# Kernel optimization log

Measured on AMD Instinct MI355X. Metric: run time of the kernel, lower is better.

## Reference

```python
import jax, jax.numpy as jnp
import numpy as np

NEG_SLOPE = 0.2
EPS = 1e-16  # PyG softmax denominator epsilon


def gat_conv(x, src, dst, W, att_src, att_dst, bias, concat):
    """One PyG-style GATConv layer (eval mode, self-loops already in src/dst).
    x: [N, F_in]; src/dst: [E]; W: [F_in, H*C]; att_*: [H, C]; bias: [H*C] or [C].
    """
    N = x.shape[0]
    H, C = att_src.shape
    h = (x @ W).reshape(N, H, C)                        # [N,H,C]
    a_s = jnp.sum(h * att_src[None], axis=-1)           # [N,H]
    a_d = jnp.sum(h * att_dst[None], axis=-1)           # [N,H]
    alpha = jax.nn.leaky_relu(a_s[src] + a_d[dst], NEG_SLOPE)  # [E,H]
    # segment softmax over incoming edges of each destination node
    m = jax.ops.segment_max(alpha, dst, num_segments=N)        # [N,H]
    alpha = jnp.exp(alpha - m[dst])
    denom = jax.ops.segment_sum(alpha, dst, num_segments=N)    # [N,H]
    alpha = alpha / (denom[dst] + EPS)
    # attention dropout is identity in eval mode
    out = jax.ops.segment_sum(h[src] * alpha[:, :, None], dst, num_segments=N)  # [N,H,C]
    out = out.reshape(N, H * C) if concat else out.mean(axis=1)
    return out + bias


def setup_inputs() -> dict:
    key = jax.random.key(0)
    ks = jax.random.split(key, 10)
    N, E, F_in, H, C1, F_out = 100000, 1600000, 128, 4, 32, 64
    hid = H * C1
    x = jax.random.normal(ks[0], (N, F_in), dtype=jnp.float32)
    edge_index = jax.random.randint(ks[1], (2, E), 0, N, dtype=jnp.int64)
    s = 1.0 / np.sqrt(F_in)
    W1 = jax.random.uniform(ks[2], (F_in, hid), minval=-s, maxval=s, dtype=jnp.float32)
    att_src1 = jax.random.normal(ks[3], (H, C1), dtype=jnp.float32) * 0.1
    att_dst1 = jax.random.normal(ks[4], (H, C1), dtype=jnp.float32) * 0.1
    b1 = jnp.zeros((hid,), dtype=jnp.float32)
    s2 = 1.0 / np.sqrt(hid)
    W2 = jax.random.uniform(ks[5], (hid, F_out), minval=-s2, maxval=s2, dtype=jnp.float32)
    att_src2 = jax.random.normal(ks[6], (1, F_out), dtype=jnp.float32) * 0.1
    att_dst2 = jax.random.normal(ks[7], (1, F_out), dtype=jnp.float32) * 0.1
    b2 = jnp.zeros((F_out,), dtype=jnp.float32)
    return {"x": x, "edge_index": edge_index,
            "W1": W1, "att_src1": att_src1, "att_dst1": att_dst1, "b1": b1,
            "W2": W2, "att_src2": att_src2, "att_dst2": att_dst2, "b2": b2}


def reference(x, edge_index, W1, att_src1, att_dst1, b1, W2, att_src2, att_dst2, b2):
    N = x.shape[0]
    loops = jnp.arange(N, dtype=edge_index.dtype)
    src = jnp.concatenate([edge_index[0], loops])  # add_self_loops=True (PyG default)
    dst = jnp.concatenate([edge_index[1], loops])
    h = gat_conv(x, src, dst, W1, att_src1, att_dst1, b1, concat=True)
    h = jax.nn.relu(h)  # dropout is identity in eval mode
    return gat_conv(h, src, dst, W2, att_src2, att_dst2, b2, concat=False)
```

## Files before the change

### kernel.cpp

```cpp
#include <hip/hip_runtime.h>
#include <hip/hip_bf16.h>

#define DEV static __device__ __forceinline__

typedef __attribute__((ext_vector_type(4))) float f32x4;
typedef __attribute__((ext_vector_type(8))) short bf16x8;
typedef __attribute__((ext_vector_type(8))) _Float16 half8;
typedef __attribute__((ext_vector_type(2))) _Float16 half2v;
typedef __attribute__((ext_vector_type(8))) unsigned short u16x8;

DEV float leakys(float v) { return v > 0.f ? v : 0.2f * v; }
DEV float4 add4(float4 a, float4 b) { return make_float4(a.x+b.x, a.y+b.y, a.z+b.z, a.w+b.w); }
DEV float4 leaky4(float4 v) { return make_float4(leakys(v.x), leakys(v.y), leakys(v.z), leakys(v.w)); }
DEV float4 exp4(float4 v) { return make_float4(__expf(v.x), __expf(v.y), __expf(v.z), __expf(v.w)); }
DEV float pick4(float4 v, int i) {
    float r = v.x;
    r = (i == 1) ? v.y : r;
    r = (i == 2) ? v.z : r;
    r = (i == 3) ? v.w : r;
    return r;
}

DEV ushort f2bf(float f) {
    union { float f; unsigned u; } v; v.f = f;
    unsigned u = v.u;
    unsigned r = (u + 0x7FFFu + ((u >> 16) & 1u)) >> 16;
    return (ushort)r;
}
DEV float bf2f(ushort h) {
    union { unsigned u; float f; } v; v.u = ((unsigned)h) << 16;
    return v.f;
}
DEV ushort f2h(float f) {
    union { _Float16 h; ushort u; } v;
    v.h = (_Float16)f;
    return v.u;
}
DEV half2v u2h2(ushort2 u) {
    union { ushort2 u; half2v h; } v; v.u = u;
    return v.h;
}

__global__ void prep_w(const float* __restrict__ W, ushort* __restrict__ Wth,
                       ushort* __restrict__ Wtl, int NC) {
    int i = blockIdx.x * 256 + threadIdx.x;
    if (i >= 128 * NC) return;
    int k = i / NC, n = i % NC;
    float v = W[i];
    ushort hi = f2bf(v);
    ushort lo = f2bf(v - bf2f(hi));
    Wth[n * 128 + k] = hi;
    Wtl[n * 128 + k] = lo;
}

template <int NCOLS, bool AH>
__launch_bounds__(256, 2)
__global__ void gemm_mfma(const float* __restrict__ A, const ushort* __restrict__ A16,
                          const ushort* __restrict__ Wth, const ushort* __restrict__ Wtl,
                          ushort* __restrict__ C16,
                          const float* __restrict__ att_s, const float* __restrict__ att_d,
                          float* __restrict__ as_out, float* __restrict__ ad_out, int N) {
    constexpr int NT = NCOLS / 64;
    __shared__ ushort Xhi[64 * 128];
    __shared__ ushort Xlo[64 * 128];
    __shared__ float pbs[64][4];
    __shared__ float pbd[64][4];
    const int t = threadIdx.x;
    const int wv = t >> 6, l = t & 63;
    const int l15 = l & 15, lhi = l >> 4;
    const int row0 = blockIdx.x * 64;
    const int n0 = wv * 16 * NT;

    if constexpr (!AH) {
        for (int i = t; i < 2048; i += 256) {
            int r = i >> 5, c4 = i & 31;
            int gr = row0 + r;
            float4 v = make_float4(0.f, 0.f, 0.f, 0.f);
            if (gr < N) v = ((const float4*)A)[(size_t)gr * 32 + c4];
            ushort4 hi, lo;
            hi.x = f2bf(v.x); lo.x = f2bf(v.x - bf2f(hi.x));
            hi.y = f2bf(v.y); lo.y = f2bf(v.y - bf2f(hi.y));
            hi.z = f2bf(v.z); lo.z = f2bf(v.z - bf2f(hi.z));
            hi.w = f2bf(v.w); lo.w = f2bf(v.w - bf2f(hi.w));
            int idx = (r * 128 + c4 * 4) ^ ((r & 7) << 3);
            *(ushort4*)&Xhi[idx] = hi;
            *(ushort4*)&Xlo[idx] = lo;
        }
    } else {
        for (int i = t; i < 1024; i += 256) {
            int r = i >> 4, c8 = i & 15;
            int gr = row0 + r;
            half8 v = (half8){0, 0, 0, 0, 0, 0, 0, 0};
            if (gr < N) v = *(const half8*)&A16[(size_t)gr * 128 + c8 * 8];
            u16x8 hi, lo;
#pragma unroll
            for (int j = 0; j < 8; j++) {
                float f = (float)v[j];
                ushort hb = f2bf(f);
                hi[j] = hb;
                lo[j] = f2bf(f - bf2f(hb));
            }
            int idx = (r * 128 + c8 * 8) ^ ((r & 7) << 3);
            *(u16x8*)&Xhi[idx] = hi;
            *(u16x8*)&Xlo[idx] = lo;
        }
    }
    __syncthreads();

    f32x4 acc[4][NT];
#pragma unroll
    for (int mt = 0; mt < 4; mt++)
#pragma unroll
        for (int nt = 0; nt < NT; nt++) acc[mt][nt] = (f32x4){0.f, 0.f, 0.f, 0.f};

#pragma unroll
    for (int ks = 0; ks < 4; ks++) {
        bf16x8 ah[4], al[4];
#pragma unroll
        for (int mt = 0; mt < 4; mt++) {
            int row = mt * 16 + l15;
            int idx = (row * 128 + ks * 32 + lhi * 8) ^ ((row & 7) << 3);
            ah[mt] = *(const bf16x8*)&Xhi[idx];
            al[mt] = *(const bf16x8*)&Xlo[idx];
        }
#pragma unroll
        for (int nt = 0; nt < NT; nt++) {
            size_t wo = (size_t)(n0 + nt * 16 + l15) * 128 + ks * 32 + lhi * 8;
            bf16x8 bh = *(const bf16x8*)&Wth[wo];
            bf16x8 bl = *(const bf16x8*)&Wtl[wo];
#pragma unroll
            for (int mt = 0; mt < 4; mt++) {
                acc[mt][nt] = __builtin_amdgcn_mfma_f32_16x16x32_bf16(ah[mt], bh, acc[mt][nt], 0, 0, 0);
                acc[mt][nt] = __builtin_amdgcn_mfma_f32_16x16x32_bf16(ah[mt], bl, acc[mt][nt], 0, 0, 0);
                acc[mt][nt] = __builtin_amdgcn_mfma_f32_16x16x32_bf16(al[mt], bh, acc[mt][nt], 0, 0, 0);
            }
        }
    }
#pragma unroll
    for (int mt = 0; mt < 4; mt++) {
#pragma unroll
        for (int j = 0; j < 4; j++) {
            int gr = row0 + mt * 16 + lhi * 4 + j;
            if (gr < N) {
#pragma unroll
                for (int nt = 0; nt < NT; nt++)
                    C16[(size_t)gr * NCOLS + n0 + nt * 16 + l15] = f2h(acc[mt][nt][j]);
            }
        }
    }
    if constexpr (NT == 2) {
        float as0 = att_s[n0 + l15],       ad0 = att_d[n0 + l15];
        float as1v = att_s[n0 + 16 + l15], ad1v = att_d[n0 + 16 + l15];
#pragma unroll
        for (int mt = 0; mt < 4; mt++) {
#pragma unroll
            for (int j = 0; j < 4; j++) {
                float ps = acc[mt][0][j] * as0 + acc[mt][1][j] * as1v;
                float pd = acc[mt][0][j] * ad0 + acc[mt][1][j] * ad1v;
#pragma unroll
                for (int o = 1; o < 16; o <<= 1) {
                    ps += __shfl_xor(ps, o);
                    pd += __shfl_xor(pd, o);
                }
                if (l15 == 0) {
                    int gr = row0 + mt * 16 + lhi * 4 + j;
                    if (gr < N) {
                        as_out[gr * 4 + wv] = ps;
                        ad_out[gr * 4 + wv] = pd;
                    }
                }
            }
        }
    } else {
        float as0 = att_s[n0 + l15], ad0 = att_d[n0 + l15];
#pragma unroll
        for (int mt = 0; mt < 4; mt++) {
#pragma unroll
            for (int j = 0; j < 4; j++) {
                float ps = acc[mt][0][j] * as0;
                float pd = acc[mt][0][j] * ad0;
#pragma unroll
                for (int o = 1; o < 16; o <<= 1) {
                    ps += __shfl_xor(ps, o);
                    pd += __shfl_xor(pd, o);
                }
                if (l15 == 0) {
                    int rl = mt * 16 + lhi * 4 + j;
                    pbs[rl][wv] = ps;
                    pbd[rl][wv] = pd;
                }
            }
        }
        __syncthreads();
        if (t < 64) {
            int gr = row0 + t;
            if (gr < N) {
                as_out[gr] = pbs[t][0] + pbs[t][1] + pbs[t][2] + pbs[t][3];
                ad_out[gr] = pbd[t][0] + pbd[t][1] + pbd[t][2] + pbd[t][3];
            }
        }
    }
}

__global__ void bcount(const int* __restrict__ dstIdx, int* __restrict__ bcounts, int E) {
    __shared__ int hist[256];
    int t = threadIdx.x;
    hist[t] = 0;
    __syncthreads();
    for (int e = blockIdx.x * 256 + t; e < E; e += gridDim.x * 256)
        atomicAdd(&hist[dstIdx[e] >> 9], 1);
    __syncthreads();
    int h = hist[t];
    if (h) atomicAdd(&bcounts[t], h);
}

__global__ void bscan(const int* __restrict__ bcounts, int* __restrict__ bbase,
                      int* __restrict__ bcursor, int NB) {
    __shared__ int lds[256];
    int t = threadIdx.x;
    int v = (t < NB) ? bcounts[t] : 0;
    lds[t] = v;
    __syncthreads();
    int val = v;
    for (int o = 1; o < 256; o <<= 1) {
        int other = (t >= o) ? lds[t - o] : 0;
        __syncthreads();
        val += other; lds[t] = val;
        __syncthreads();
    }
    if (t < NB) { bbase[t] = val - v; bcursor[t] = val - v; }
}

__global__ void bscatter(const int* __restrict__ srcIdx, const int* __restrict__ dstIdx,
                         int* __restrict__ bcursor, uint2* __restrict__ ebuf, int E) {
    __shared__ int hist[256];
    __shared__ int gofs[256];
    int t = threadIdx.x;
    hist[t] = 0;
    __syncthreads();
    int e0 = blockIdx.x * 4096;
    int e1 = min(E, e0 + 4096);
    for (int e = e0 + t; e < e1; e += 256)
        atomicAdd(&hist[dstIdx[e] >> 9], 1);
    __syncthreads();
    int h = hist[t];
    if (h) gofs[t] = atomicAdd(&bcursor[t], h);
    __syncthreads();
    hist[t] = 0;
    __syncthreads();
    for (int e = e0 + t; e < e1; e += 256) {
        int d = dstIdx[e];
        int b = d >> 9;
        int r = atomicAdd(&hist[b], 1);
        uint2 v; v.x = (unsigned)srcIdx[e]; v.y = (unsigned)d;
        ebuf[gofs[b] + r] = v;
    }
}

__global__ void bfill(const uint2* __restrict__ ebuf, const int* __restrict__ bbase,
                      int* __restrict__ rowptr, int* __restrict__ esrc,
                      int N, int NB, int E) {
    __shared__ int cnt[512];
    __shared__ int lds[256];
    int b = blockIdx.x, t = threadIdx.x;
    int n0 = b << 9;
    cnt[t] = 0; cnt[t + 256] = 0;
    __syncthreads();
    int e0 = bbase[b];
    int e1 = (b + 1 < NB) ? bbase[b + 1] : E;
    for (int e = e0 + t; e < e1; e += 256)
        atomicAdd(&cnt[ebuf[e].y & 511], 1);
    __syncthreads();
    int c0 = cnt[2 * t], c1 = cnt[2 * t + 1];
    int s = c0 + c1;
    lds[t] = s;
    __syncthreads();
    int val = s;
    for (int o = 1; o < 256; o <<= 1) {
        int other = (t >= o) ? lds[t - o] : 0;
        __syncthreads();
        val += other; lds[t] = val;
        __syncthreads();
    }
    int p = val - s;
    int nrem = N - n0;
    if (2 * t < nrem)     rowptr[n0 + 2 * t]     = e0 + p;
    if (2 * t + 1 < nrem) rowptr[n0 + 2 * t + 1] = e0 + p + c0;
    cnt[2 * t] = p; cnt[2 * t + 1] = p + c0;
    __syncthreads();
    for (int e = e0 + t; e < e1; e += 256) {
        uint2 ed = ebuf[e];
        int r = atomicAdd(&cnt[ed.y & 511], 1);
        esrc[e0 + r] = (int)ed.x;
    }
    if (b == 0 && t == 0) rowptr[N] = E;
}

__launch_bounds__(256)
__global__ void aggregate1(const ushort* __restrict__ h16,
                           const float* __restrict__ as1, const float* __restrict__ ad1,
                           const int* __restrict__ rowptr, const int* __restrict__ esrc,
                           const float* __restrict__ b1, ushort* __restrict__ out1h, int N) {
    __shared__ ushort wbuf[4][4 * 72];
    __shared__ int    sbuf[4][16];
    int wid = threadIdx.x >> 6, lane = threadIdx.x & 63;
    int node = blockIdx.x * 4 + wid;
    if (node >= N) return;
    float4 asn = *(const float4*)&as1[node * 4];
    float4 adn = *(const float4*)&ad1[node * 4];
    float4 selfw = exp4(leaky4(add4(asn, adn)));
    int start = rowptr[node], end = rowptr[node + 1];

    int eidx = lane & 15, hd = lane >> 4;
    float adh1 = pick4(adn, hd);
    int q = lane >> 4, c = lane & 15;
    int hh = c >> 2;
    float esum = 0.f;
    float acc[8] = {0.f, 0.f, 0.f, 0.f, 0.f, 0.f, 0.f, 0.f};

    for (int base = start; base < end; base += 16) {
        int cnt = end - base; if (cnt > 16) cnt = 16;
        int s = 0; float w = 0.f;
        if (eidx < cnt) {
            s = esrc[base + eidx];
            w = __expf(leakys(as1[s * 4 + hd] + adh1));
        }
        esum += w;
        wbuf[wid][hd * 72 + eidx] = f2h(w);
        if (hd == 0) sbuf[wid][eidx] = s;
#pragma unroll
        for (int i = 0; i < cnt; i += 8) {
            int i1 = i + 2 * q;
            int2 ss = *(const int2*)&sbuf[wid][i1];
            half2v wp = u2h2(*(const ushort2*)&wbuf[wid][hh * 72 + i1]);
            half8 hv1 = *(const half8*)&h16[(size_t)ss.x * 128 + c * 8];
            half8 hv2 = *(const half8*)&h16[(size_t)ss.y * 128 + c * 8];
#pragma unroll
            for (int j = 0; j < 8; j++) {
                half2v hp = {hv1[j], hv2[j]};
                acc[j] = __builtin_amdgcn_fdot2(hp, wp, acc[j], false);
            }
        }
    }
#pragma unroll
    for (int o = 1; o < 16; o <<= 1) esum += __shfl_xor(esum, o);
    float denom = __shfl(esum, hh << 4) + pick4(selfw, hh) + 1e-16f;
    float inv = 1.f / denom;
    float sw = pick4(selfw, hh);

#pragma unroll
    for (int j = 0; j < 8; j++) {
        acc[j] += __shfl_xor(acc[j], 16);
        acc[j] += __shfl_xor(acc[j], 32);
    }
    if (q == 0) {
        half8 hs = *(const half8*)&h16[(size_t)node * 128 + c * 8];
        const float* bb = &b1[c * 8];
        half8 ov;
#pragma unroll
        for (int j = 0; j < 8; j++) {
            float oj = fmaxf((acc[j] + sw * (float)hs[j]) * inv + bb[j], 0.f);
            ov[j] = (_Float16)oj;
        }
        *(half8*)&out1h[(size_t)node * 128 + c * 8] = ov;
    }
}

__launch_bounds__(256)
__global__ void aggregate2(const ushort* __restrict__ h16,
                           const float* __restrict__ as2, const float* __restrict__ ad2,
                           const int* __restrict__ rowptr, const int* __restrict__ esrc,
                           const float* __restrict__ b2, float* __restrict__ out, int N) {
    __shared__ ushort wbuf[4][64];
    __shared__ int    sbuf[4][64];
    int wid = threadIdx.x >> 6, lane = threadIdx.x & 63;
    int node = blockIdx.x * 4 + wid;
    if (node >= N) return;
    float adn = ad2[node];
    float selfw = __expf(leakys(as2[node] + adn));
    int start = rowptr[node], end = rowptr[node + 1];

    int q = lane >> 3, c = lane & 7;
    float ssum = 0.f;
    float acc[8] = {0.f, 0.f, 0.f, 0.f, 0.f, 0.f, 0.f, 0.f};

    for (int base = start; base < end; base += 64) {
        int cnt = end - base; if (cnt > 64) cnt = 64;
        int s = 0; float w = 0.f;
        if (lane < cnt) {
            s = esrc[base + lane];
            w = __expf(leakys(as2[s] + adn));
        }
        ssum += w;
        wbuf[wid][lane] = f2h(w);
        sbuf[wid][lane] = s;
#pragma unroll 2
        for (int i = 0; i < cnt; i += 16) {
            int i1 = i + 2 * q;
            int2 ss = *(const int2*)&sbuf[wid][i1];
            half2v wp = u2h2(*(const ushort2*)&wbuf[wid][i1]);
            half8 hv1 = *(const half8*)&h16[(size_t)ss.x * 64 + c * 8];
            half8 hv2 = *(const half8*)&h16[(size_t)ss.y * 64 + c * 8];
#pragma unroll
            for (int j = 0; j < 8; j++) {
                half2v hp = {hv1[j], hv2[j]};
                acc[j] = __builtin_amdgcn_fdot2(hp, wp, acc[j], false);
            }
        }
    }
#pragma unroll
    for (int o = 1; o < 64; o <<= 1) ssum += __shfl_xor(ssum, o);
    float inv = 1.f / (ssum + selfw + 1e-16f);

#pragma unroll
    for (int j = 0; j < 8; j++) {
        acc[j] += __shfl_xor(acc[j], 8);
        acc[j] += __shfl_xor(acc[j], 16);
        acc[j] += __shfl_xor(acc[j], 32);
    }
    if (lane < 8) {
        half8 hs = *(const half8*)&h16[(size_t)node * 64 + c * 8];
        const float* bb = &b2[c * 8];
        float o[8];
#pragma unroll
        for (int j = 0; j < 8; j++)
            o[j] = (acc[j] + selfw * (float)hs[j]) * inv + bb[j];
        float4* op = (float4*)&out[(size_t)node * 64 + c * 8];
        op[0] = make_float4(o[0], o[1], o[2], o[3]);
        op[1] = make_float4(o[4], o[5], o[6], o[7]);
    }
}

extern "C" void kernel_launch(void* const* d_in, const int* in_sizes, int n_in,
                              void* d_out, int out_size, void* d_ws, size_t ws_size,
                              hipStream_t stream) {
    const float* x      = (const float*)d_in[0];
    const int*   ei     = (const int*)d_in[1];
    const float* W1     = (const float*)d_in[2];
    const float* att_s1 = (const float*)d_in[3];
    const float* att_d1 = (const float*)d_in[4];
    const float* b1     = (const float*)d_in[5];
    const float* W2     = (const float*)d_in[6];
    const float* att_s2 = (const float*)d_in[7];
    const float* att_d2 = (const float*)d_in[8];
    const float* b2     = (const float*)d_in[9];

    const int N = in_sizes[0] / 128;
    const int E = in_sizes[1] / 2;
    const int NB = (N + 511) >> 9;

    char* ws = (char*)d_ws;
    size_t off = 0;
    auto alloc = [&](size_t bytes) -> void* {
        off = (off + 255) & ~(size_t)255;
        void* p = ws + off;
        off += bytes;
        return p;
    };
    ushort* h16   = (ushort*)alloc((size_t)N * 128 * 2);
    ushort* out1h = (ushort*)alloc((size_t)N * 128 * 2);
    float* as1    = (float*)alloc((size_t)N * 4 * 4);
    float* ad1    = (float*)alloc((size_t)N * 4 * 4);
    float* as2    = (float*)alloc((size_t)N * 4);
    float* ad2    = (float*)alloc((size_t)N * 4);
    int*   rowptr = (int*)alloc((size_t)(N + 1) * 4);
    int*   esrc   = (int*)alloc((size_t)E * 4);
    int*   bcounts = (int*)alloc(256 * 4);
    int*   bbase   = (int*)alloc(256 * 4);
    int*   bcursor = (int*)alloc(256 * 4);
    ushort* Wt1h  = (ushort*)alloc(128 * 128 * 2);
    ushort* Wt1l  = (ushort*)alloc(128 * 128 * 2);
    ushort* Wt2h  = (ushort*)alloc(64 * 128 * 2);
    ushort* Wt2l  = (ushort*)alloc(64 * 128 * 2);
    ushort* h16b = h16;
    uint2* ebuf = (uint2*)out1h;

    const int* srcIdx = ei;
    const int* dstIdx = ei + E;

    hipMemsetAsync(bcounts, 0, 256 * 4, stream);

    prep_w<<<64, 256, 0, stream>>>(W1, Wt1h, Wt1l, 128);
    prep_w<<<32, 256, 0, stream>>>(W2, Wt2h, Wt2l, 64);

    gemm_mfma<128, false><<<(N + 63) / 64, 256, 0, stream>>>(
        x, nullptr, Wt1h, Wt1l, h16, att_s1, att_d1, as1, ad1, N);

    bcount<<<1024, 256, 0, stream>>>(dstIdx, bcounts, E);
    bscan<<<1, 256, 0, stream>>>(bcounts, bbase, bcursor, NB);
    bscatter<<<(E + 4095) / 4096, 256, 0, stream>>>(srcIdx, dstIdx, bcursor, ebuf, E);
    bfill<<<NB, 256, 0, stream>>>(ebuf, bbase, rowptr, esrc, N, NB, E);

    aggregate1<<<(N + 3) / 4, 256, 0, stream>>>(h16, as1, ad1, rowptr, esrc,
                                                b1, out1h, N);

    gemm_mfma<64, true><<<(N + 63) / 64, 256, 0, stream>>>(
        nullptr, out1h, Wt2h, Wt2l, h16b, att_s2, att_d2, as2, ad2, N);

    aggregate2<<<(N + 3) / 4, 256, 0, stream>>>(h16b, as2, ad2, rowptr, esrc,
                                                b2, (float*)d_out, N);
}
```

Baseline: 262.1 us.

## Fuse dst-bucket histogram into first GEMM launch; widen aggregate1 edge batches

Extra blocks appended to the first GEMM grid now compute the destination-bucket histogram, so the separate bcount launch is removed and the histogram runs alongside the GEMM. aggregate1 now handles 32 edges per iteration instead of 16, with smaller padded LDS buffers, which issues more gather loads per batch. aggregate2's inner-loop unroll goes from 2 to 4. The histogram blocks share the GEMM's LDS allocation and launch bounds, which can limit occupancy, and their __syncthreads sits inside a block-uniform branch, so it is safe.

Result: faster. 246.7 us (-5.9%).

```diff
diff --git a/kernel.cpp b/kernel.cpp
--- a/kernel.cpp
+++ b/kernel.cpp
@@ -59,13 +59,29 @@
                           const ushort* __restrict__ Wth, const ushort* __restrict__ Wtl,
                           ushort* __restrict__ C16,
                           const float* __restrict__ att_s, const float* __restrict__ att_d,
-                          float* __restrict__ as_out, float* __restrict__ ad_out, int N) {
+                          float* __restrict__ as_out, float* __restrict__ ad_out, int N,
+                          const int* __restrict__ dstIdx, int* __restrict__ bcounts,
+                          int E, int nGemmBlocks) {
     constexpr int NT = NCOLS / 64;
     __shared__ ushort Xhi[64 * 128];
     __shared__ ushort Xlo[64 * 128];
     __shared__ float pbs[64][4];
     __shared__ float pbd[64][4];
     const int t = threadIdx.x;
+
+    if (blockIdx.x >= nGemmBlocks) {
+        __shared__ int hist[256];
+        hist[t] = 0;
+        __syncthreads();
+        int nb = gridDim.x - nGemmBlocks;
+        for (int e = (blockIdx.x - nGemmBlocks) * 256 + t; e < E; e += nb * 256)
+            atomicAdd(&hist[dstIdx[e] >> 9], 1);
+        __syncthreads();
+        int h = hist[t];
+        if (h) atomicAdd(&bcounts[t], h);
+        return;
+    }
+
     const int wv = t >> 6, l = t & 63;
     const int l15 = l & 15, lhi = l >> 4;
     const int row0 = blockIdx.x * 64;
@@ -202,18 +218,6 @@
     }
 }
 
-__global__ void bcount(const int* __restrict__ dstIdx, int* __restrict__ bcounts, int E) {
-    __shared__ int hist[256];
-    int t = threadIdx.x;
-    hist[t] = 0;
-    __syncthreads();
-    for (int e = blockIdx.x * 256 + t; e < E; e += gridDim.x * 256)
-        atomicAdd(&hist[dstIdx[e] >> 9], 1);
-    __syncthreads();
-    int h = hist[t];
-    if (h) atomicAdd(&bcounts[t], h);
-}
-
 __global__ void bscan(const int* __restrict__ bcounts, int* __restrict__ bbase,
                       int* __restrict__ bcursor, int NB) {
     __shared__ int lds[256];
@@ -301,8 +305,8 @@
                            const float* __restrict__ as1, const float* __restrict__ ad1,
                            const int* __restrict__ rowptr, const int* __restrict__ esrc,
                            const float* __restrict__ b1, ushort* __restrict__ out1h, int N) {
-    __shared__ ushort wbuf[4][4 * 72];
-    __shared__ int    sbuf[4][16];
+    __shared__ ushort wbuf[4][4 * 40];
+    __shared__ int    sbuf[4][32];
     int wid = threadIdx.x >> 6, lane = threadIdx.x & 63;
     int node = blockIdx.x * 4 + wid;
     if (node >= N) return;
@@ -318,21 +322,23 @@
     float esum = 0.f;
     float acc[8] = {0.f, 0.f, 0.f, 0.f, 0.f, 0.f, 0.f, 0.f};
 
-    for (int base = start; base < end; base += 16) {
-        int cnt = end - base; if (cnt > 16) cnt = 16;
-        int s = 0; float w = 0.f;
-        if (eidx < cnt) {
-            s = esrc[base + eidx];
-            w = __expf(leakys(as1[s * 4 + hd] + adh1));
-        }
-        esum += w;
-        wbuf[wid][hd * 72 + eidx] = f2h(w);
-        if (hd == 0) sbuf[wid][eidx] = s;
-#pragma unroll
+    for (int base = start; base < end; base += 32) {
+        int cnt = end - base; if (cnt > 32) cnt = 32;
+        int e1i = eidx, e2i = eidx + 16;
+        int s1 = 0, s2 = 0; float w1 = 0.f, w2 = 0.f;
+        if (e1i < cnt) s1 = esrc[base + e1i];
+        if (e2i < cnt) s2 = esrc[base + e2i];
+        if (e1i < cnt) w1 = __expf(leakys(as1[s1 * 4 + hd] + adh1));
+        if (e2i < cnt) w2 = __expf(leakys(as1[s2 * 4 + hd] + adh1));
+        esum += w1 + w2;
+        wbuf[wid][hd * 40 + e1i] = f2h(w1);
+        wbuf[wid][hd * 40 + e2i] = f2h(w2);
+        if (hd == 0) { sbuf[wid][e1i] = s1; sbuf[wid][e2i] = s2; }
+#pragma unroll 4
         for (int i = 0; i < cnt; i += 8) {
             int i1 = i + 2 * q;
             int2 ss = *(const int2*)&sbuf[wid][i1];
-            half2v wp = u2h2(*(const ushort2*)&wbuf[wid][hh * 72 + i1]);
+            half2v wp = u2h2(*(const ushort2*)&wbuf[wid][hh * 40 + i1]);
             half8 hv1 = *(const half8*)&h16[(size_t)ss.x * 128 + c * 8];
             half8 hv2 = *(const half8*)&h16[(size_t)ss.y * 128 + c * 8];
 #pragma unroll
@@ -394,7 +400,7 @@
         ssum += w;
         wbuf[wid][lane] = f2h(w);
         sbuf[wid][lane] = s;
-#pragma unroll 2
+#pragma unroll 4
         for (int i = 0; i < cnt; i += 16) {
             int i1 = i + 2 * q;
             int2 ss = *(const int2*)&sbuf[wid][i1];
@@ -483,10 +489,11 @@
     prep_w<<<64, 256, 0, stream>>>(W1, Wt1h, Wt1l, 128);
     prep_w<<<32, 256, 0, stream>>>(W2, Wt2h, Wt2l, 64);
 
-    gemm_mfma<128, false><<<(N + 63) / 64, 256, 0, stream>>>(
-        x, nullptr, Wt1h, Wt1l, h16, att_s1, att_d1, as1, ad1, N);
-
-    bcount<<<1024, 256, 0, stream>>>(dstIdx, bcounts, E);
+    const int nGemm1 = (N + 63) / 64;
+    gemm_mfma<128, false><<<nGemm1 + 512, 256, 0, stream>>>(
+        x, nullptr, Wt1h, Wt1l, h16, att_s1, att_d1, as1, ad1, N,
+        dstIdx, bcounts, E, nGemm1);
+
     bscan<<<1, 256, 0, stream>>>(bcounts, bbase, bcursor, NB);
     bscatter<<<(E + 4095) / 4096, 256, 0, stream>>>(srcIdx, dstIdx, bcursor, ebuf, E);
     bfill<<<NB, 256, 0, stream>>>(ebuf, bbase, rowptr, esrc, N, NB, E);
@@ -494,8 +501,10 @@
     aggregate1<<<(N + 3) / 4, 256, 0, stream>>>(h16, as1, ad1, rowptr, esrc,
                                                 b1, out1h, N);
 
-    gemm_mfma<64, true><<<(N + 63) / 64, 256, 0, stream>>>(
-        nullptr, out1h, Wt2h, Wt2l, h16b, att_s2, att_d2, as2, ad2, N);
+    const int nGemm2 = (N + 63) / 64;
+    gemm_mfma<64, true><<<nGemm2, 256, 0, stream>>>(
+        nullptr, out1h, Wt2h, Wt2l, h16b, att_s2, att_d2, as2, ad2, N,
+        nullptr, nullptr, 0, nGemm2);
 
     aggregate2<<<(N + 3) / 4, 256, 0, stream>>>(h16b, as2, ad2, rowptr, esrc,
                                                 b2, (float*)d_out, N);
```
